# Kernel optimization log

Measured on AMD Instinct MI355X. Metric: run time of the kernel, lower is better.

## Reference

```python
import jax, jax.numpy as jnp
import numpy as np

B, S, HID = 2, 2048, 2048
H, G = 16, 1
D = HID // H  # 128


def setup_inputs() -> dict:
    key = jax.random.key(0)
    ks = jax.random.split(key, 10)
    sc = 0.02
    inp = {
        "hidden_states": jax.random.normal(ks[0], (B, S, HID), jnp.float32),
        # 1 above the diagonal -> masked out (matches torch code: scores += mask * -1e9)
        "causal_mask": jnp.triu(jnp.ones((1, 1, S, S), jnp.float32), k=1),
        "padding_mask": jnp.zeros((B, S), jnp.float32),
        "Wq": jax.random.normal(ks[1], (HID, HID), jnp.float32) * sc,
        "bq": jnp.zeros((HID,), jnp.float32),
        "Wk": jax.random.normal(ks[2], (G * D, HID), jnp.float32) * sc,
        "bk": jnp.zeros((G * D,), jnp.float32),
        "Wv": jax.random.normal(ks[3], (G * D, HID), jnp.float32) * sc,
        "bv": jnp.zeros((G * D,), jnp.float32),
        "Wo": jax.random.normal(ks[4], (HID, HID), jnp.float32) * sc,
        "bo": jnp.zeros((HID,), jnp.float32),
    }
    return inp


def reference(hidden_states, causal_mask, padding_mask, Wq, bq, Wk, bk, Wv, bv, Wo, bo):
    b, s, _ = hidden_states.shape
    q = hidden_states @ Wq.T + bq            # [B,S,HID]
    k = hidden_states @ Wk.T + bk            # [B,S,G*D]
    v = hidden_states @ Wv.T + bv            # [B,S,G*D]
    q = q.reshape(b, s, H, D).transpose(0, 2, 1, 3)   # [B,H,S,D]
    k = k.reshape(b, s, G, D).transpose(0, 2, 1, 3)   # [B,G,S,D]
    v = v.reshape(b, s, G, D).transpose(0, 2, 1, 3)   # [B,G,S,D]
    # broadcast G=1 KV heads against H query heads (exactly what torch.matmul does)
    scores = jnp.matmul(q, jnp.swapaxes(k, -1, -2)) / jnp.sqrt(jnp.float32(D))  # [B,H,S,S]
    scores = scores + causal_mask * (-1e9)
    scores = scores + padding_mask[:, None, None, :] * (-1e9)
    weights = jax.nn.softmax(scores, axis=-1)
    out = jnp.matmul(weights, v)                       # [B,H,S,D]
    out = out.transpose(0, 2, 1, 3).reshape(b, s, H * D)
    return out @ Wo.T + bo
```

## Files before the change

kernel.cpp:

```cpp
#include <hip/hip_runtime.h>
#include <hip/hip_bf16.h>

typedef __attribute__((ext_vector_type(8))) short s8v;
typedef __attribute__((ext_vector_type(4))) float f4v;
typedef __hip_bfloat16 bf16;

#define S_LEN 2048
#define HID_DIM 2048
#define N_HEADS 16
#define HEAD_D 128
#define M_ROWS 4096
#define N_FUSED 2304

static __device__ inline short f2b_bits(float f) {
  bf16 h = __float2bfloat16(f);
  short u;
  __builtin_memcpy(&u, &h, 2);
  return u;
}

struct Cvt5 {
  const float* src[5];
  bf16* dst[5];
  long n8[5];
};

__global__ __launch_bounds__(256) void cvt_f32_bf16(Cvt5 c) {
  long i = (long)blockIdx.x * 256 + threadIdx.x;
#pragma unroll
  for (int s = 0; s < 5; ++s) {
    long n8 = c.n8[s];
    if (i < n8) {
      const float* p = c.src[s] + i * 8;
      float4 f0 = *(const float4*)p;
      float4 f1 = *(const float4*)(p + 4);
      s8v t;
      t[0] = f2b_bits(f0.x); t[1] = f2b_bits(f0.y);
      t[2] = f2b_bits(f0.z); t[3] = f2b_bits(f0.w);
      t[4] = f2b_bits(f1.x); t[5] = f2b_bits(f1.y);
      t[6] = f2b_bits(f1.z); t[7] = f2b_bits(f1.w);
      *(s8v*)(c.dst[s] + i * 8) = t;
      return;
    }
    i -= n8;
  }
}

__global__ __launch_bounds__(256) void gemm_qkv(
    const bf16* __restrict__ A, const bf16* __restrict__ Wf,
    const float* __restrict__ bq, const float* __restrict__ bk,
    const float* __restrict__ bv,
    bf16* __restrict__ qout, bf16* __restrict__ kout, bf16* __restrict__ vout) {
  __shared__ __align__(16) bf16 As[128 * 72];
  __shared__ __align__(16) bf16 Bs[128 * 72];
  const int t = threadIdx.x;
  const int lane = t & 63, wid = t >> 6;
  const int l15 = lane & 15, quad = lane >> 4;
  const int wm = wid >> 1, wn = wid & 1;
  const int bm = blockIdx.x, bn = blockIdx.y;
  f4v acc[4][4] = {};
  for (int kt = 0; kt < HID_DIM / 64; ++kt) {
    __syncthreads();
#pragma unroll
    for (int i = 0; i < 4; ++i) {
      int idx = t + i * 256;
      int row = idx >> 3, c8 = (idx & 7) * 8;
      *(uint4*)&As[row * 72 + c8] =
          *(const uint4*)&A[(size_t)(bm * 128 + row) * HID_DIM + kt * 64 + c8];
      *(uint4*)&Bs[row * 72 + c8] =
          *(const uint4*)&Wf[(size_t)(bn * 128 + row) * HID_DIM + kt * 64 + c8];
    }
    __syncthreads();
#pragma unroll
    for (int ks = 0; ks < 2; ++ks) {
      s8v af[4], bfr[4];
#pragma unroll
      for (int mi = 0; mi < 4; ++mi)
        af[mi] = *(const s8v*)&As[(wm * 64 + mi * 16 + l15) * 72 + ks * 32 + quad * 8];
#pragma unroll
      for (int ni = 0; ni < 4; ++ni)
        bfr[ni] = *(const s8v*)&Bs[(wn * 64 + ni * 16 + l15) * 72 + ks * 32 + quad * 8];
#pragma unroll
      for (int mi = 0; mi < 4; ++mi)
#pragma unroll
        for (int ni = 0; ni < 4; ++ni)
          acc[mi][ni] = __builtin_amdgcn_mfma_f32_16x16x32_bf16(af[mi], bfr[ni], acc[mi][ni], 0, 0, 0);
    }
  }
  const float* bias;
  bf16* C;
  int ldC, colbase;
  if (bn < 16)       { bias = bq; C = qout; ldC = HID_DIM; colbase = bn * 128; }
  else if (bn == 16) { bias = bk; C = kout; ldC = HEAD_D;  colbase = 0; }
  else               { bias = bv; C = vout; ldC = HEAD_D;  colbase = 0; }
#pragma unroll
  for (int ni = 0; ni < 4; ++ni) {
    int cl = wn * 64 + ni * 16 + l15;
    float bvv = bias[colbase + cl];
#pragma unroll
    for (int mi = 0; mi < 4; ++mi)
#pragma unroll
      for (int r = 0; r < 4; ++r) {
        int row = bm * 128 + wm * 64 + mi * 16 + quad * 4 + r;
        C[(size_t)row * ldC + colbase + cl] = __float2bfloat16(acc[mi][ni][r] + bvv);
      }
  }
}

template <bool WBF>
__global__ __launch_bounds__(256) void gemm_o(
    const bf16* __restrict__ A, const void* __restrict__ Wp,
    const float* __restrict__ bias, float* __restrict__ C) {
  __shared__ __align__(16) bf16 As[128 * 72];
  __shared__ __align__(16) bf16 Bs[128 * 72];
  const int t = threadIdx.x;
  const int lane = t & 63, wid = t >> 6;
  const int l15 = lane & 15, quad = lane >> 4;
  const int wm = wid >> 1, wn = wid & 1;
  const int bm = blockIdx.x, bn = blockIdx.y;
  f4v acc[4][4] = {};
  for (int kt = 0; kt < HID_DIM / 64; ++kt) {
    __syncthreads();
#pragma unroll
    for (int i = 0; i < 4; ++i) {
      int idx = t + i * 256;
      int row = idx >> 3, c8 = (idx & 7) * 8;
      *(uint4*)&As[row * 72 + c8] =
          *(const uint4*)&A[(size_t)(bm * 128 + row) * HID_DIM + kt * 64 + c8];
      if constexpr (WBF) {
        *(uint4*)&Bs[row * 72 + c8] =
            *(const uint4*)&((const bf16*)Wp)[(size_t)(bn * 128 + row) * HID_DIM + kt * 64 + c8];
      } else {
        const float* s = (const float*)Wp + (size_t)(bn * 128 + row) * HID_DIM + kt * 64 + c8;
        float4 f0 = *(const float4*)s;
        float4 f1 = *(const float4*)(s + 4);
        s8v tmp;
        tmp[0] = f2b_bits(f0.x); tmp[1] = f2b_bits(f0.y);
        tmp[2] = f2b_bits(f0.z); tmp[3] = f2b_bits(f0.w);
        tmp[4] = f2b_bits(f1.x); tmp[5] = f2b_bits(f1.y);
        tmp[6] = f2b_bits(f1.z); tmp[7] = f2b_bits(f1.w);
        *(s8v*)&Bs[row * 72 + c8] = tmp;
      }
    }
    __syncthreads();
#pragma unroll
    for (int ks = 0; ks < 2; ++ks) {
      s8v af[4], bfr[4];
#pragma unroll
      for (int mi = 0; mi < 4; ++mi)
        af[mi] = *(const s8v*)&As[(wm * 64 + mi * 16 + l15) * 72 + ks * 32 + quad * 8];
#pragma unroll
      for (int ni = 0; ni < 4; ++ni)
        bfr[ni] = *(const s8v*)&Bs[(wn * 64 + ni * 16 + l15) * 72 + ks * 32 + quad * 8];
#pragma unroll
      for (int mi = 0; mi < 4; ++mi)
#pragma unroll
        for (int ni = 0; ni < 4; ++ni)
          acc[mi][ni] = __builtin_amdgcn_mfma_f32_16x16x32_bf16(af[mi], bfr[ni], acc[mi][ni], 0, 0, 0);
    }
  }
#pragma unroll
  for (int ni = 0; ni < 4; ++ni) {
    int col = bn * 128 + wn * 64 + ni * 16 + l15;
    float bvv = bias[col];
#pragma unroll
    for (int mi = 0; mi < 4; ++mi)
#pragma unroll
      for (int r = 0; r < 4; ++r) {
        int row = bm * 128 + wm * 64 + mi * 16 + quad * 4 + r;
        C[(size_t)row * HID_DIM + col] = acc[mi][ni][r] + bvv;
      }
  }
}

__global__ __launch_bounds__(256) void attn_fwd(
    const bf16* q, const bf16* __restrict__ k,
    const bf16* __restrict__ v, bf16* o) {
  __shared__ __align__(16) bf16 Ks[64 * 136];
  __shared__ __align__(16) bf16 Vt[128 * 72];
  __shared__ __align__(16) bf16 Ps[64 * 72];
  const int t = threadIdx.x;
  const int lane = t & 63, w = t >> 6;
  const int l15 = lane & 15, quad = lane >> 4;
  const int q0 = blockIdx.x * 64;
  const int h = blockIdx.y, b = blockIdx.z;
  const size_t bs = (size_t)b * S_LEN;

  s8v qf[4];
#pragma unroll
  for (int ks = 0; ks < 4; ++ks)
    qf[ks] = *(const s8v*)&q[(bs + q0 + w * 16 + l15) * HID_DIM + h * HEAD_D + ks * 32 + quad * 8];

  float mst = -1e30f, lst = 0.f;
  f4v acco[8] = {};
  const float scale = 0.08838834764831845f;
  const int jt = q0 / 64 + 1;

  uint4 kreg[4], vreg[4];
#pragma unroll
  for (int i = 0; i < 4; ++i) {
    int idx = t + i * 256;
    kreg[i] = *(const uint4*)&k[(bs + (idx >> 4)) * HEAD_D + (idx & 15) * 8];
    vreg[i] = *(const uint4*)&v[(bs + (idx & 63)) * HEAD_D + (idx >> 6) * 8];
  }

  for (int j = 0; j < jt; ++j) {
    __syncthreads();
#pragma unroll
    for (int i = 0; i < 4; ++i) {
      int idx = t + i * 256;
      *(uint4*)&Ks[(idx >> 4) * 136 + (idx & 15) * 8] = kreg[i];
      const bf16* pv = (const bf16*)&vreg[i];
      int n = idx & 63, g = idx >> 6;
#pragma unroll
      for (int e = 0; e < 8; ++e) Vt[(g * 8 + e) * 72 + n] = pv[e];
    }
    if (j + 1 < jt) {
#pragma unroll
      for (int i = 0; i < 4; ++i) {
        int idx = t + i * 256;
        kreg[i] = *(const uint4*)&k[(bs + (j + 1) * 64 + (idx >> 4)) * HEAD_D + (idx & 15) * 8];
        vreg[i] = *(const uint4*)&v[(bs + (j + 1) * 64 + (idx & 63)) * HEAD_D + (idx >> 6) * 8];
      }
    }
    __syncthreads();

    f4v accs[4] = {};
#pragma unroll
    for (int ks = 0; ks < 4; ++ks) {
      s8v kf[4];
#pragma unroll
      for (int ni = 0; ni < 4; ++ni)
        kf[ni] = *(const s8v*)&Ks[(ni * 16 + l15) * 136 + ks * 32 + quad * 8];
#pragma unroll
      for (int ni = 0; ni < 4; ++ni)
        accs[ni] = __builtin_amdgcn_mfma_f32_16x16x32_bf16(kf[ni], qf[ks], accs[ni], 0, 0, 0);
    }

    const int mg = q0 + w * 16 + l15;
    const bool full = (j * 64 + 63 <= q0 + w * 16);
    float sv[4][4];
    float tmax = -1e30f;
#pragma unroll
    for (int ni = 0; ni < 4; ++ni)
#pragma unroll
      for (int r = 0; r < 4; ++r) {
        int ng = j * 64 + ni * 16 + quad * 4 + r;
        float s = accs[ni][r] * scale;
        if (!full && ng > mg) s = -1e30f;
        sv[ni][r] = s;
        tmax = fmaxf(tmax, s);
      }
    tmax = fmaxf(tmax, __shfl_xor(tmax, 16, 64));
    tmax = fmaxf(tmax, __shfl_xor(tmax, 32, 64));
    float mnew = fmaxf(mst, tmax);
    float alpha = __expf(mst - mnew);
    float psum = 0.f;
#pragma unroll
    for (int ni = 0; ni < 4; ++ni) {
      float p0 = __expf(sv[ni][0] - mnew);
      float p1 = __expf(sv[ni][1] - mnew);
      float p2 = __expf(sv[ni][2] - mnew);
      float p3 = __expf(sv[ni][3] - mnew);
      psum += (p0 + p1) + (p2 + p3);
      uint2 packed;
      packed.x = (unsigned)(unsigned short)f2b_bits(p0) | ((unsigned)(unsigned short)f2b_bits(p1) << 16);
      packed.y = (unsigned)(unsigned short)f2b_bits(p2) | ((unsigned)(unsigned short)f2b_bits(p3) << 16);
      *(uint2*)&Ps[(w * 16 + l15) * 72 + ni * 16 + quad * 4] = packed;
    }
    psum += __shfl_xor(psum, 16, 64);
    psum += __shfl_xor(psum, 32, 64);
    lst = lst * alpha + psum;
    mst = mnew;
#pragma unroll
    for (int r = 0; r < 4; ++r) {
      float ar = __shfl(alpha, quad * 4 + r, 64);
#pragma unroll
      for (int di = 0; di < 8; ++di) acco[di][r] *= ar;
    }

#pragma unroll
    for (int ks = 0; ks < 2; ++ks) {
      s8v pf = *(const s8v*)&Ps[(w * 16 + l15) * 72 + ks * 32 + quad * 8];
      s8v vf[8];
#pragma unroll
      for (int di = 0; di < 8; ++di)
        vf[di] = *(const s8v*)&Vt[(di * 16 + l15) * 72 + ks * 32 + quad * 8];
#pragma unroll
      for (int di = 0; di < 8; ++di)
        acco[di] = __builtin_amdgcn_mfma_f32_16x16x32_bf16(pf, vf[di], acco[di], 0, 0, 0);
    }
  }

#pragma unroll
  for (int r = 0; r < 4; ++r) {
    float lr = __shfl(lst, quad * 4 + r, 64);
    float rinv = 1.0f / lr;
    size_t row = bs + q0 + w * 16 + quad * 4 + r;
#pragma unroll
    for (int di = 0; di < 8; ++di)
      o[row * HID_DIM + h * HEAD_D + di * 16 + l15] = __float2bfloat16(acco[di][r] * rinv);
  }
}

extern "C" void kernel_launch(void* const* d_in, const int* in_sizes, int n_in,
                              void* d_out, int out_size, void* d_ws, size_t ws_size,
                              hipStream_t stream) {
  const float* hs = (const float*)d_in[0];
  const float* Wq = (const float*)d_in[3];
  const float* bq = (const float*)d_in[4];
  const float* Wk = (const float*)d_in[5];
  const float* bk = (const float*)d_in[6];
  const float* Wv = (const float*)d_in[7];
  const float* bv = (const float*)d_in[8];
  const float* Wo = (const float*)d_in[9];
  const float* bo = (const float*)d_in[10];
  float* out = (float*)d_out;

  bf16* qab = (bf16*)d_ws;
  const bool big_ws = ws_size >= (size_t)25 * 1024 * 1024;
  bf16* wob = (bf16*)((char*)d_ws + (size_t)16 * 1024 * 1024);

  char* ob = (char*)d_out;
  bf16* wqkvb = (bf16*)ob;
  bf16* kb = (bf16*)(ob + (size_t)9437184);
  bf16* vb = (bf16*)(ob + (size_t)9437184 + 1048576);
  bf16* hsb = (bf16*)(ob + (size_t)9437184 + 2097152);

  Cvt5 c;
  c.src[0] = hs; c.dst[0] = hsb;
  c.n8[0] = (long)M_ROWS * HID_DIM / 8;
  c.src[1] = Wq; c.dst[1] = wqkvb;
  c.n8[1] = (long)HID_DIM * HID_DIM / 8;
  c.src[2] = Wk; c.dst[2] = wqkvb + (size_t)HID_DIM * HID_DIM;
  c.n8[2] = (long)HEAD_D * HID_DIM / 8;
  c.src[3] = Wv; c.dst[3] = wqkvb + (size_t)(HID_DIM + HEAD_D) * HID_DIM;
  c.n8[3] = (long)HEAD_D * HID_DIM / 8;
  c.src[4] = Wo; c.dst[4] = big_ws ? wob : (bf16*)nullptr;
  c.n8[4] = big_ws ? (long)HID_DIM * HID_DIM / 8 : 0;
  long total8 = c.n8[0] + c.n8[1] + c.n8[2] + c.n8[3] + c.n8[4];

  cvt_f32_bf16<<<dim3((unsigned)((total8 + 255) / 256)), dim3(256), 0, stream>>>(c);
  gemm_qkv<<<dim3(M_ROWS / 128, N_FUSED / 128), dim3(256), 0, stream>>>(
      hsb, wqkvb, bq, bk, bv, qab, kb, vb);
  attn_fwd<<<dim3(S_LEN / 64, N_HEADS, 2), dim3(256), 0, stream>>>(qab, kb, vb, qab);
  if (big_ws)
    gemm_o<true><<<dim3(M_ROWS / 128, HID_DIM / 128), dim3(256), 0, stream>>>(qab, wob, bo, out);
  else
    gemm_o<false><<<dim3(M_ROWS / 128, HID_DIM / 128), dim3(256), 0, stream>>>(qab, Wo, bo, out);
}
```

Baseline: 437.0 us.

## Store V transposed from QKV GEMM and read K/V directly in attention

The QKV GEMM epilogue now writes V in transposed [D, B*S] layout, so attention can load V fragments from global memory without an LDS transpose. The attention kernel drops K/V shared-memory staging and barriers, reading K and V^T directly from global memory (shared across heads through cache since G=1). Each block now covers 128 query rows, each wave 32 rows, and the grid is issued in reverse so the longest causal tiles start first. Softmax uses exp2 with a folded scale and packed bf16 conversion. The risks are uncoalesced strided V^T stores in the GEMM and higher global/L2 traffic for the unshared K/V loads.

```diff
diff --git a/kernel.cpp b/kernel.cpp
--- a/kernel.cpp
+++ b/kernel.cpp
@@ -12,10 +12,19 @@
 #define M_ROWS 4096
 #define N_FUSED 2304
 
+#define EXP2F(x) __builtin_amdgcn_exp2f(x)
+
 static __device__ inline short f2b_bits(float f) {
   bf16 h = __float2bfloat16(f);
   short u;
   __builtin_memcpy(&u, &h, 2);
+  return u;
+}
+
+static __device__ inline unsigned pk_bf16(float a, float b) {
+  __hip_bfloat162 h2 = __float22bfloat162_rn(float2{a, b});
+  unsigned u;
+  __builtin_memcpy(&u, &h2, 4);
   return u;
 }
 
@@ -50,7 +59,7 @@
     const bf16* __restrict__ A, const bf16* __restrict__ Wf,
     const float* __restrict__ bq, const float* __restrict__ bk,
     const float* __restrict__ bv,
-    bf16* __restrict__ qout, bf16* __restrict__ kout, bf16* __restrict__ vout) {
+    bf16* __restrict__ qout, bf16* __restrict__ kout, bf16* __restrict__ vtout) {
   __shared__ __align__(16) bf16 As[128 * 72];
   __shared__ __align__(16) bf16 Bs[128 * 72];
   const int t = threadIdx.x;
@@ -87,23 +96,45 @@
           acc[mi][ni] = __builtin_amdgcn_mfma_f32_16x16x32_bf16(af[mi], bfr[ni], acc[mi][ni], 0, 0, 0);
     }
   }
-  const float* bias;
-  bf16* C;
-  int ldC, colbase;
-  if (bn < 16)       { bias = bq; C = qout; ldC = HID_DIM; colbase = bn * 128; }
-  else if (bn == 16) { bias = bk; C = kout; ldC = HEAD_D;  colbase = 0; }
-  else               { bias = bv; C = vout; ldC = HEAD_D;  colbase = 0; }
-#pragma unroll
-  for (int ni = 0; ni < 4; ++ni) {
-    int cl = wn * 64 + ni * 16 + l15;
-    float bvv = bias[colbase + cl];
-#pragma unroll
-    for (int mi = 0; mi < 4; ++mi)
-#pragma unroll
-      for (int r = 0; r < 4; ++r) {
-        int row = bm * 128 + wm * 64 + mi * 16 + quad * 4 + r;
-        C[(size_t)row * ldC + colbase + cl] = __float2bfloat16(acc[mi][ni][r] + bvv);
-      }
+  if (bn < 16) {
+#pragma unroll
+    for (int ni = 0; ni < 4; ++ni) {
+      int cl = wn * 64 + ni * 16 + l15;
+      float bvv = bq[bn * 128 + cl];
+#pragma unroll
+      for (int mi = 0; mi < 4; ++mi)
+#pragma unroll
+        for (int r = 0; r < 4; ++r) {
+          int row = bm * 128 + wm * 64 + mi * 16 + quad * 4 + r;
+          qout[(size_t)row * HID_DIM + bn * 128 + cl] = __float2bfloat16(acc[mi][ni][r] + bvv);
+        }
+    }
+  } else if (bn == 16) {
+#pragma unroll
+    for (int ni = 0; ni < 4; ++ni) {
+      int cl = wn * 64 + ni * 16 + l15;
+      float bvv = bk[cl];
+#pragma unroll
+      for (int mi = 0; mi < 4; ++mi)
+#pragma unroll
+        for (int r = 0; r < 4; ++r) {
+          int row = bm * 128 + wm * 64 + mi * 16 + quad * 4 + r;
+          kout[(size_t)row * HEAD_D + cl] = __float2bfloat16(acc[mi][ni][r] + bvv);
+        }
+    }
+  } else {
+#pragma unroll
+    for (int ni = 0; ni < 4; ++ni) {
+      int cl = wn * 64 + ni * 16 + l15;
+      float bvv = bv[cl];
+#pragma unroll
+      for (int mi = 0; mi < 4; ++mi)
+#pragma unroll
+        for (int r = 0; r < 4; ++r) {
+          int row = bm * 128 + wm * 64 + mi * 16 + quad * 4 + r;
+          vtout[(size_t)cl * M_ROWS + row] = __float2bfloat16(acc[mi][ni][r] + bvv);
+        }
+    }
   }
 }
 
@@ -175,132 +206,119 @@
 
 __global__ __launch_bounds__(256) void attn_fwd(
     const bf16* q, const bf16* __restrict__ k,
-    const bf16* __restrict__ v, bf16* o) {
-  __shared__ __align__(16) bf16 Ks[64 * 136];
-  __shared__ __align__(16) bf16 Vt[128 * 72];
-  __shared__ __align__(16) bf16 Ps[64 * 72];
+    const bf16* __restrict__ vt, bf16* o) {
+  __shared__ __align__(16) bf16 Ps[128 * 72];
   const int t = threadIdx.x;
   const int lane = t & 63, w = t >> 6;
   const int l15 = lane & 15, quad = lane >> 4;
-  const int q0 = blockIdx.x * 64;
+  const int qi = (S_LEN / 128 - 1) - blockIdx.x;
+  const int q0 = qi * 128;
   const int h = blockIdx.y, b = blockIdx.z;
   const size_t bs = (size_t)b * S_LEN;
-
-  s8v qf[4];
-#pragma unroll
-  for (int ks = 0; ks < 4; ++ks)
-    qf[ks] = *(const s8v*)&q[(bs + q0 + w * 16 + l15) * HID_DIM + h * HEAD_D + ks * 32 + quad * 8];
-
-  float mst = -1e30f, lst = 0.f;
-  f4v acco[8] = {};
-  const float scale = 0.08838834764831845f;
-  const int jt = q0 / 64 + 1;
-
-  uint4 kreg[4], vreg[4];
-#pragma unroll
-  for (int i = 0; i < 4; ++i) {
-    int idx = t + i * 256;
-    kreg[i] = *(const uint4*)&k[(bs + (idx >> 4)) * HEAD_D + (idx & 15) * 8];
-    vreg[i] = *(const uint4*)&v[(bs + (idx & 63)) * HEAD_D + (idx >> 6) * 8];
-  }
-
+  const int r0 = q0 + w * 32;
+
+  s8v qf[2][4];
+#pragma unroll
+  for (int mi = 0; mi < 2; ++mi)
+#pragma unroll
+    for (int ks = 0; ks < 4; ++ks)
+      qf[mi][ks] = *(const s8v*)&q[(bs + r0 + mi * 16 + l15) * HID_DIM + h * HEAD_D + ks * 32 + quad * 8];
+
+  float mst[2] = {-1e30f, -1e30f};
+  float lst[2] = {0.f, 0.f};
+  f4v acco[2][8] = {};
+  const float scale2 = 0.12754245f;
+
+  const int jt = (r0 + 31) / 64 + 1;
   for (int j = 0; j < jt; ++j) {
-    __syncthreads();
-#pragma unroll
-    for (int i = 0; i < 4; ++i) {
-      int idx = t + i * 256;
-      *(uint4*)&Ks[(idx >> 4) * 136 + (idx & 15) * 8] = kreg[i];
-      const bf16* pv = (const bf16*)&vreg[i];
-      int n = idx & 63, g = idx >> 6;
-#pragma unroll
-      for (int e = 0; e < 8; ++e) Vt[(g * 8 + e) * 72 + n] = pv[e];
-    }
-    if (j + 1 < jt) {
-#pragma unroll
-      for (int i = 0; i < 4; ++i) {
-        int idx = t + i * 256;
-        kreg[i] = *(const uint4*)&k[(bs + (j + 1) * 64 + (idx >> 4)) * HEAD_D + (idx & 15) * 8];
-        vreg[i] = *(const uint4*)&v[(bs + (j + 1) * 64 + (idx & 63)) * HEAD_D + (idx >> 6) * 8];
-      }
-    }
-    __syncthreads();
-
-    f4v accs[4] = {};
+    f4v accs[4][2] = {};
 #pragma unroll
     for (int ks = 0; ks < 4; ++ks) {
       s8v kf[4];
 #pragma unroll
       for (int ni = 0; ni < 4; ++ni)
-        kf[ni] = *(const s8v*)&Ks[(ni * 16 + l15) * 136 + ks * 32 + quad * 8];
-#pragma unroll
-      for (int ni = 0; ni < 4; ++ni)
-        accs[ni] = __builtin_amdgcn_mfma_f32_16x16x32_bf16(kf[ni], qf[ks], accs[ni], 0, 0, 0);
-    }
-
-    const int mg = q0 + w * 16 + l15;
-    const bool full = (j * 64 + 63 <= q0 + w * 16);
-    float sv[4][4];
-    float tmax = -1e30f;
-#pragma unroll
-    for (int ni = 0; ni < 4; ++ni)
+        kf[ni] = *(const s8v*)&k[(bs + j * 64 + ni * 16 + l15) * HEAD_D + ks * 32 + quad * 8];
+#pragma unroll
+      for (int ni = 0; ni < 4; ++ni)
+#pragma unroll
+        for (int mi = 0; mi < 2; ++mi)
+          accs[ni][mi] = __builtin_amdgcn_mfma_f32_16x16x32_bf16(kf[ni], qf[mi][ks], accs[ni][mi], 0, 0, 0);
+    }
+
+#pragma unroll
+    for (int mi = 0; mi < 2; ++mi) {
+      const int mg = r0 + mi * 16 + l15;
+      const bool full = (j * 64 + 63 <= r0 + mi * 16);
+      float sv[4][4];
+      float tmax = -1e30f;
+#pragma unroll
+      for (int ni = 0; ni < 4; ++ni)
+#pragma unroll
+        for (int r = 0; r < 4; ++r) {
+          int ng = j * 64 + ni * 16 + quad * 4 + r;
+          float s = accs[ni][mi][r];
+          if (!full && ng > mg) s = -1e30f;
+          sv[ni][r] = s;
+          tmax = fmaxf(tmax, s);
+        }
+      tmax = fmaxf(tmax, __shfl_xor(tmax, 16, 64));
+      tmax = fmaxf(tmax, __shfl_xor(tmax, 32, 64));
+      float mnew = fmaxf(mst[mi], tmax);
+      float nms = -mnew * scale2;
+      float alpha = EXP2F(fmaf(mst[mi], scale2, nms));
+      float psum = 0.f;
+#pragma unroll
+      for (int ni = 0; ni < 4; ++ni) {
+        float p0 = EXP2F(fmaf(sv[ni][0], scale2, nms));
+        float p1 = EXP2F(fmaf(sv[ni][1], scale2, nms));
+        float p2 = EXP2F(fmaf(sv[ni][2], scale2, nms));
+        float p3 = EXP2F(fmaf(sv[ni][3], scale2, nms));
+        psum += (p0 + p1) + (p2 + p3);
+        uint2 packed;
+        packed.x = pk_bf16(p0, p1);
+        packed.y = pk_bf16(p2, p3);
+        *(uint2*)&Ps[(w * 32 + mi * 16 + l15) * 72 + ni * 16 + quad * 4] = packed;
+      }
+      psum += __shfl_xor(psum, 16, 64);
+      psum += __shfl_xor(psum, 32, 64);
+      lst[mi] = lst[mi] * alpha + psum;
+      mst[mi] = mnew;
 #pragma unroll
       for (int r = 0; r < 4; ++r) {
-        int ng = j * 64 + ni * 16 + quad * 4 + r;
-        float s = accs[ni][r] * scale;
-        if (!full && ng > mg) s = -1e30f;
-        sv[ni][r] = s;
-        tmax = fmaxf(tmax, s);
+        float ar = __shfl(alpha, quad * 4 + r, 64);
+#pragma unroll
+        for (int di = 0; di < 8; ++di) acco[mi][di][r] *= ar;
       }
-    tmax = fmaxf(tmax, __shfl_xor(tmax, 16, 64));
-    tmax = fmaxf(tmax, __shfl_xor(tmax, 32, 64));
-    float mnew = fmaxf(mst, tmax);
-    float alpha = __expf(mst - mnew);
-    float psum = 0.f;
-#pragma unroll
-    for (int ni = 0; ni < 4; ++ni) {
-      float p0 = __expf(sv[ni][0] - mnew);
-      float p1 = __expf(sv[ni][1] - mnew);
-      float p2 = __expf(sv[ni][2] - mnew);
-      float p3 = __expf(sv[ni][3] - mnew);
-      psum += (p0 + p1) + (p2 + p3);
-      uint2 packed;
-      packed.x = (unsigned)(unsigned short)f2b_bits(p0) | ((unsigned)(unsigned short)f2b_bits(p1) << 16);
-      packed.y = (unsigned)(unsigned short)f2b_bits(p2) | ((unsigned)(unsigned short)f2b_bits(p3) << 16);
-      *(uint2*)&Ps[(w * 16 + l15) * 72 + ni * 16 + quad * 4] = packed;
-    }
-    psum += __shfl_xor(psum, 16, 64);
-    psum += __shfl_xor(psum, 32, 64);
-    lst = lst * alpha + psum;
-    mst = mnew;
+    }
+
+#pragma unroll
+    for (int ks = 0; ks < 2; ++ks) {
+      s8v pf[2], vf[8];
+#pragma unroll
+      for (int mi = 0; mi < 2; ++mi)
+        pf[mi] = *(const s8v*)&Ps[(w * 32 + mi * 16 + l15) * 72 + ks * 32 + quad * 8];
+#pragma unroll
+      for (int di = 0; di < 8; ++di)
+        vf[di] = *(const s8v*)&vt[(size_t)(di * 16 + l15) * M_ROWS + bs + j * 64 + ks * 32 + quad * 8];
+#pragma unroll
+      for (int mi = 0; mi < 2; ++mi)
+#pragma unroll
+        for (int di = 0; di < 8; ++di)
+          acco[mi][di] = __builtin_amdgcn_mfma_f32_16x16x32_bf16(pf[mi], vf[di], acco[mi][di], 0, 0, 0);
+    }
+  }
+
+#pragma unroll
+  for (int mi = 0; mi < 2; ++mi)
 #pragma unroll
     for (int r = 0; r < 4; ++r) {
-      float ar = __shfl(alpha, quad * 4 + r, 64);
-#pragma unroll
-      for (int di = 0; di < 8; ++di) acco[di][r] *= ar;
-    }
-
-#pragma unroll
-    for (int ks = 0; ks < 2; ++ks) {
-      s8v pf = *(const s8v*)&Ps[(w * 16 + l15) * 72 + ks * 32 + quad * 8];
-      s8v vf[8];
+      float lr = __shfl(lst[mi], quad * 4 + r, 64);
+      float rinv = 1.0f / lr;
+      size_t row = bs + r0 + mi * 16 + quad * 4 + r;
 #pragma unroll
       for (int di = 0; di < 8; ++di)
-        vf[di] = *(const s8v*)&Vt[(di * 16 + l15) * 72 + ks * 32 + quad * 8];
-#pragma unroll
-      for (int di = 0; di < 8; ++di)
-        acco[di] = __builtin_amdgcn_mfma_f32_16x16x32_bf16(pf, vf[di], acco[di], 0, 0, 0);
-    }
-  }
-
-#pragma unroll
-  for (int r = 0; r < 4; ++r) {
-    float lr = __shfl(lst, quad * 4 + r, 64);
-    float rinv = 1.0f / lr;
-    size_t row = bs + q0 + w * 16 + quad * 4 + r;
-#pragma unroll
-    for (int di = 0; di < 8; ++di)
-      o[row * HID_DIM + h * HEAD_D + di * 16 + l15] = __float2bfloat16(acco[di][r] * rinv);
-  }
+        o[row * HID_DIM + h * HEAD_D + di * 16 + l15] = __float2bfloat16(acco[mi][di][r] * rinv);
+    }
 }
 
 extern "C" void kernel_launch(void* const* d_in, const int* in_sizes, int n_in,
@@ -324,7 +342,7 @@
   char* ob = (char*)d_out;
   bf16* wqkvb = (bf16*)ob;
   bf16* kb = (bf16*)(ob + (size_t)9437184);
-  bf16* vb = (bf16*)(ob + (size_t)9437184 + 1048576);
+  bf16* vtb = (bf16*)(ob + (size_t)9437184 + 1048576);
   bf16* hsb = (bf16*)(ob + (size_t)9437184 + 2097152);
 
   Cvt5 c;
@@ -342,8 +360,8 @@
 
   cvt_f32_bf16<<<dim3((unsigned)((total8 + 255) / 256)), dim3(256), 0, stream>>>(c);
   gemm_qkv<<<dim3(M_ROWS / 128, N_FUSED / 128), dim3(256), 0, stream>>>(
-      hsb, wqkvb, bq, bk, bv, qab, kb, vb);
-  attn_fwd<<<dim3(S_LEN / 64, N_HEADS, 2), dim3(256), 0, stream>>>(qab, kb, vb, qab);
+      hsb, wqkvb, bq, bk, bv, qab, kb, vtb);
+  attn_fwd<<<dim3(S_LEN / 128, N_HEADS, 2), dim3(256), 0, stream>>>(qab, kb, vtb, qab);
   if (big_ws)
     gemm_o<true><<<dim3(M_ROWS / 128, HID_DIM / 128), dim3(256), 0, stream>>>(qab, wob, bo, out);
   else
```

Result: slower. 474.2 us (+8.5%).
